# Optimization experiments

Hardware: AMD Instinct MI355X
Metric: run time of the kernel (lower is better)

## Reference

```python
import jax, jax.numpy as jnp
import numpy as np

B = 128          # batch size
N_KG = 500       # KG vertices
N = N_KG + 2     # + sensor node + zero target node
D = 1024         # embed_dim (hard-coded in forward)
H = 256          # gnn_hidden
E = 4000         # edges
EPS = 1e-5


def setup_inputs() -> dict:
    key = jax.random.key(0)
    ks = jax.random.split(key, 8)
    return {
        "sensor_batch": jax.random.normal(ks[0], (B, D), jnp.float32),
        "base_vertices": jax.random.normal(ks[1], (N_KG, D), jnp.float32),
        "edge_index": jax.random.randint(ks[2], (2, E), 0, N, jnp.int64),
        "W1": jax.random.normal(ks[3], (D, H), jnp.float32) * (1.0 / np.sqrt(D)),
        "b1": jnp.zeros((H,), jnp.float32),
        "gamma1": jnp.ones((H,), jnp.float32),
        "beta1": jnp.zeros((H,), jnp.float32),
        "W2": jax.random.normal(ks[4], (H, H), jnp.float32) * (1.0 / np.sqrt(H)),
        "b2": jnp.zeros((H,), jnp.float32),
        "gamma2": jnp.ones((H,), jnp.float32),
        "beta2": jnp.zeros((H,), jnp.float32),
        "W3": jax.random.normal(ks[5], (H, H), jnp.float32) * (1.0 / np.sqrt(H)),
        "b3": jnp.zeros((H,), jnp.float32),
        "gamma3": jnp.ones((H,), jnp.float32),
        "beta3": jnp.zeros((H,), jnp.float32),
    }


def _gcn_norm(edge_index):
    # add self loops, symmetric normalization D^{-1/2} A D^{-1/2}
    loops = jnp.arange(N, dtype=edge_index.dtype)
    src = jnp.concatenate([edge_index[0], loops])
    dst = jnp.concatenate([edge_index[1], loops])
    deg = jnp.zeros((N,), jnp.float32).at[dst].add(1.0)
    dinv = jnp.where(deg > 0, jax.lax.rsqrt(deg), 0.0)
    norm = dinv[src] * dinv[dst]   # [E+N]
    return src, dst, norm


def _gcn_conv(x, W, b, src, dst, norm):
    # x: [B, N, F_in] -> [B, N, F_out]
    h = jnp.einsum('bnf,fh->bnh', x, W)
    msg = h[:, src, :] * norm[None, :, None]            # gather + scale
    out = jnp.zeros_like(h).at[:, dst, :].add(msg)      # scatter-add
    return out + b


def _bn_elu(x, gamma, beta):
    # BatchNorm1d over flattened (B*N, H) in training mode, then ELU
    Bn, Nn, Hh = x.shape
    xf = x.reshape(Bn * Nn, Hh)
    mean = jnp.mean(xf, axis=0)
    var = jnp.mean(jnp.square(xf - mean), axis=0)  # biased, as in torch BN fwd
    y = (xf - mean) * jax.lax.rsqrt(var + EPS) * gamma + beta
    return jax.nn.elu(y).reshape(Bn, Nn, Hh)


def reference(sensor_batch, base_vertices, edge_index,
              W1, b1, gamma1, beta1,
              W2, b2, gamma2, beta2,
              W3, b3, gamma3, beta3):
    Bn = sensor_batch.shape[0]
    # x = [base_vertices; sensor_input; zeros] per batch element -> [B, N, D]
    base = jnp.broadcast_to(base_vertices[None], (Bn, N_KG, D))
    zeros = jnp.zeros((Bn, 1, D), sensor_batch.dtype)
    x = jnp.concatenate([base, sensor_batch[:, None, :], zeros], axis=1)

    src, dst, norm = _gcn_norm(edge_index)
    x = _bn_elu(_gcn_conv(x, W1, b1, src, dst, norm), gamma1, beta1)
    x = _bn_elu(_gcn_conv(x, W2, b2, src, dst, norm), gamma2, beta2)
    x = _bn_elu(_gcn_conv(x, W3, b3, src, dst, norm), gamma3, beta3)
    return x
```

## Files before the change

kernel.cpp:

```cpp
#include <hip/hip_runtime.h>
#include <cstdint>
#include <cstddef>

#define NNODES 502
#define NKG    500
#define NPAD   512
#define NEDGE  4000
#define NET    4502
#define BB     128
#define DD     1024
#define HH     256
#define MROWS  (BB*NNODES)
#define MT     65536
#define MCAT   628
#define EPITCH 136

typedef short short8 __attribute__((ext_vector_type(8)));
typedef float f32x4  __attribute__((ext_vector_type(4)));

__device__ __forceinline__ unsigned short f2bf(float f) {
  union { float f; unsigned int u; } v; v.f = f;
  unsigned int r = v.u + 0x7fffu + ((v.u >> 16) & 1u);
  return (unsigned short)(r >> 16);
}

__device__ __forceinline__ float bf2f(unsigned short u) {
  union { unsigned int u; float f; } v; v.u = ((unsigned int)u) << 16;
  return v.f;
}

__device__ __forceinline__ float elu(float y) {
  return (y > 0.f) ? y : (__expf(y) - 1.f);
}

__device__ __forceinline__ void stage16(const void* g, void* l) {
  __builtin_amdgcn_global_load_lds((__attribute__((address_space(1))) void*)g,
                                   (__attribute__((address_space(3))) void*)l, 16, 0, 0);
}

__device__ __forceinline__ void mfma16(f32x4& c, short8 a, short8 b) {
  asm volatile("v_mfma_f32_16x16x32_bf16 %0, %1, %2, %0" : "+v"(c) : "v"(a), "v"(b));
}

__device__ inline void get_edge(const int* __restrict__ e, int i, int i64mode,
                                int& src, int& dst) {
  if (i < NEDGE) {
    if (i64mode) { src = e[2*i]; dst = e[2*NEDGE + 2*i]; }
    else         { src = e[i];   dst = e[NEDGE + i]; }
  } else {
    src = dst = i - NEDGE;
  }
  src = min(max(src, 0), NNODES-1);
  dst = min(max(dst, 0), NNODES-1);
}

__device__ __forceinline__ int detect_mode(const int* __restrict__ e) {
  __shared__ int sflag;
  if (threadIdx.x == 0) sflag = 0;
  __syncthreads();
  if (e[2*threadIdx.x + 1] != 0) atomicOr(&sflag, 1);
  __syncthreads();
  return sflag == 0;
}

__global__ void deg_kernel(const int* __restrict__ e, int* __restrict__ deg) {
  int i64 = detect_mode(e);
  int i = blockIdx.x*256 + threadIdx.x;
  if (i >= NET) return;
  int src, dst; get_edge(e, i, i64, src, dst);
  atomicAdd(&deg[dst], 1);
}

__global__ void scan_kernel(const int* __restrict__ deg, float* __restrict__ dinv,
                            int* __restrict__ rp, int* __restrict__ cursor) {
  __shared__ int s[512];
  int t = threadIdx.x;
  int cnt = (t < NNODES) ? deg[t] : 0;
  s[t] = cnt;
  if (t < NNODES) dinv[t] = rsqrtf((float)cnt);
  __syncthreads();
  for (int off = 1; off < 512; off <<= 1) {
    int v = (t >= off) ? s[t-off] : 0;
    __syncthreads();
    s[t] += v;
    __syncthreads();
  }
  if (t == 0) rp[0] = 0;
  if (t < NNODES) { rp[t+1] = s[t]; cursor[t] = s[t] - cnt; }
}

__global__ void fillsdf_kernel(const int* __restrict__ e, const float* __restrict__ dinv,
                               int* __restrict__ cursor, int* __restrict__ colA,
                               float* __restrict__ valA, float* __restrict__ Sdf) {
  int i64 = detect_mode(e);
  int i = blockIdx.x*256 + threadIdx.x;
  if (i >= NET) return;
  int src, dst; get_edge(e, i, i64, src, dst);
  float v = dinv[src] * dinv[dst];
  int pos = atomicAdd(&cursor[dst], 1);
  colA[pos] = src;
  valA[pos] = v;
  atomicAdd(&Sdf[dst*NPAD + src], v);
}

__global__ void sdcvt_kernel(const float* __restrict__ Sdf, unsigned short* __restrict__ Sd) {
  int i = blockIdx.x*256 + threadIdx.x;
  Sd[i] = f2bf(Sdf[i]);
}

__global__ __launch_bounds__(256) void prep_kernel(
    const float* __restrict__ W1, const float* __restrict__ W2, const float* __restrict__ W3,
    const float* __restrict__ base, const float* __restrict__ sensor,
    unsigned short* __restrict__ Wt1, unsigned short* __restrict__ Wt2,
    unsigned short* __restrict__ Wt3, unsigned short* __restrict__ Xp1,
    float* __restrict__ hcatz) {
  int bid = blockIdx.x, tid = threadIdx.x;
  if (bid < 512) {
    const float* W = (bid & 256) ? W3 : W2;
    unsigned short* Wt = (bid & 256) ? Wt3 : Wt2;
    int n = bid & 255;
    Wt[n*HH + tid] = f2bf(W[(size_t)tid*HH + n]);
  } else if (bid < 768) {
    int n = bid - 512;
    for (int k = tid; k < DD; k += 256)
      Wt1[n*DD + k] = f2bf(W1[(size_t)k*HH + n]);
  } else if (bid < 1408) {
    int i = (bid - 768)*256 + tid;
    int r = i >> 8, c = (i & 255) * 4;
    float4 v = make_float4(0.f, 0.f, 0.f, 0.f);
    if (r < NKG) v = *(const float4*)&base[(size_t)r*DD + c];
    else if (r < MCAT) v = *(const float4*)&sensor[(size_t)(r-NKG)*DD + c];
    union { unsigned short u[4]; uint2 d; } p;
    p.u[0]=f2bf(v.x); p.u[1]=f2bf(v.y); p.u[2]=f2bf(v.z); p.u[3]=f2bf(v.w);
    *(uint2*)&Xp1[(size_t)r*DD + c] = p.d;
  } else {
    hcatz[(bid - 1408)*256 + tid] = 0.f;
  }
}

__global__ __launch_bounds__(256) void gemm1m_kernel(
    const unsigned short* __restrict__ Ag,
    const unsigned short* __restrict__ Bg,
    float* __restrict__ C) {
  __shared__ unsigned short As[128*32];
  __shared__ unsigned short Bs[128*32];
  int tid = threadIdx.x;
  int wave = tid >> 6, lane = tid & 63;
  int l15 = lane & 15, quad = lane >> 4;
  int wm = (wave & 1) * 64, wn = (wave >> 1) * 64;
  int row0 = blockIdx.y * 128, col0 = blockIdx.x * 128;
  int kbase = blockIdx.z * 256;
  f32x4 acc[4][4] = {};
  for (int k0 = kbase; k0 < kbase + 256; k0 += 32) {
#pragma unroll
    for (int q = 0; q < 2; ++q) {
      int c = wave*128 + q*64 + lane;
      stage16(Ag + (size_t)(row0 + (c>>2))*DD + k0 + (c&3)*8, As + c*8);
      stage16(Bg + (size_t)(col0 + (c>>2))*DD + k0 + (c&3)*8, Bs + c*8);
    }
    __syncthreads();
    short8 af[4], bfv[4];
#pragma unroll
    for (int i = 0; i < 4; ++i) {
      af[i]  = *(const short8*)(As + (wm + i*16 + l15)*32 + quad*8);
      bfv[i] = *(const short8*)(Bs + (wn + i*16 + l15)*32 + quad*8);
    }
#pragma unroll
    for (int mi = 0; mi < 4; ++mi)
#pragma unroll
      for (int ni = 0; ni < 4; ++ni)
        mfma16(acc[mi][ni], af[mi], bfv[ni]);
    __syncthreads();
  }
  asm volatile("s_nop 7\n\ts_nop 7" ::);
#pragma unroll
  for (int ni = 0; ni < 4; ++ni) {
    int n = col0 + wn + ni*16 + l15;
#pragma unroll
    for (int mi = 0; mi < 4; ++mi) {
      int m = row0 + wm + mi*16 + quad*4;
#pragma unroll
      for (int r = 0; r < 4; ++r)
        if (m + r < MCAT) atomicAdd(&C[(size_t)(m+r)*HH + n], acc[mi][ni][r]);
    }
  }
}

__global__ void ac_kernel(const int* __restrict__ rp, const int* __restrict__ colA,
                          const float* __restrict__ valA, const float* __restrict__ hcat,
                          float* __restrict__ Abuf, float* __restrict__ cbuf) {
  int n = blockIdx.x, h = threadIdx.x;
  int s = rp[n], e = rp[n+1];
  float acc = 0.f, cacc = 0.f;
  for (int t = s; t < e; ++t) {
    int cl = colA[t]; float v = valA[t];
    if (cl < NKG) acc += v * hcat[cl*HH + h];
    else if (cl == NKG) cacc += v;
  }
  Abuf[n*HH + h] = acc;
  if (h == 0) cbuf[n] = cacc;
}

__global__ __launch_bounds__(256) void bn1n_kernel(
    const float* __restrict__ Abuf, const float* __restrict__ cbuf,
    const float* __restrict__ hcat,
    float* __restrict__ sA1, float* __restrict__ sAA1, float* __restrict__ sAc1,
    float* __restrict__ scp, float* __restrict__ ssA, float* __restrict__ sssA) {
  int bid = blockIdx.x, h = threadIdx.x;
  if (bid < 32) {
    int n0 = bid*16, n1 = min(n0+16, NNODES);
    float sA = 0, sAA = 0, sAc = 0, sc = 0, scc = 0;
    for (int n = n0; n < n1; ++n) {
      float a = Abuf[n*HH + h]; float cn = cbuf[n];
      sA += a; sAA += a*a; sAc += a*cn; sc += cn; scc += cn*cn;
    }
    atomicAdd(&sA1[h], sA); atomicAdd(&sAA1[h], sAA); atomicAdd(&sAc1[h], sAc);
    if (h == 0) { atomicAdd(&scp[0], sc); atomicAdd(&scp[1], scc); }
  } else {
    int b0 = (bid-32)*16;
    float ss = 0, sss = 0;
    for (int b = b0; b < b0+16; ++b) {
      float v = hcat[(size_t)(NKG + b)*HH + h]; ss += v; sss += v*v;
    }
    atomicAdd(&ssA[h], ss); atomicAdd(&sssA[h], sss);
  }
}

__global__ void fin1_kernel(const float* __restrict__ sA1, const float* __restrict__ sAA1,
                            const float* __restrict__ sAc1, const float* __restrict__ scp,
                            const float* __restrict__ ssA, const float* __restrict__ sssA,
                            const float* __restrict__ gamma, const float* __restrict__ beta,
                            float* __restrict__ scale, float* __restrict__ shift) {
  int h = threadIdx.x;
  float sA = sA1[h], sAA = sAA1[h], sAc = sAc1[h];
  float sc = scp[0], scc = scp[1];
  float ss = ssA[h], sss = sssA[h];
  const float cnt = (float)MROWS;
  float mean = ((float)BB * sA + sc*ss) / cnt;
  float msq  = ((float)BB * sAA + 2.f*sAc*ss + scc*sss) / cnt;
  float var  = msq - mean*mean;
  float scl  = gamma[h] * rsqrtf(var + 1e-5f);
  scale[h] = scl; shift[h] = beta[h] - mean*scl;
}

__global__ __launch_bounds__(256) void x2_kernel(
    const float* __restrict__ Abuf, const float* __restrict__ cbuf,
    const float* __restrict__ hcat, const float* __restrict__ scale,
    const float* __restrict__ shift, unsigned short* __restrict__ Xb) {
  int idx = blockIdx.x*256 + threadIdx.x;
  int row = idx >> 6, h0 = (idx & 63)*4;
  int b = row >> 9, n = row & (NPAD-1);
  union { unsigned short u[4]; uint2 d; } p;
  p.d = make_uint2(0,0);
  if (n < NNODES) {
    float4 a  = *(const float4*)(Abuf + n*HH + h0);
    float4 s  = *(const float4*)(hcat + (size_t)(NKG + b)*HH + h0);
    float4 sc = *(const float4*)(scale + h0);
    float4 sh = *(const float4*)(shift + h0);
    float cn = cbuf[n];
    p.u[0] = f2bf(elu((a.x + cn*s.x)*sc.x + sh.x));
    p.u[1] = f2bf(elu((a.y + cn*s.y)*sc.y + sh.y));
    p.u[2] = f2bf(elu((a.z + cn*s.z)*sc.z + sh.z));
    p.u[3] = f2bf(elu((a.w + cn*s.w)*sc.w + sh.w));
  }
  *(uint2*)(Xb + (size_t)row*HH + h0) = p.d;
}

template<int FBN>
__global__ __launch_bounds__(256) void gemmT2_kernel(
    const unsigned short* __restrict__ Ag,
    const unsigned short* __restrict__ Bg,
    const float* __restrict__ sums, const float* __restrict__ ssqs,
    const float* __restrict__ gamma, const float* __restrict__ beta,
    unsigned short* __restrict__ Tt) {
  __shared__ __align__(16) unsigned short smem[25600];
  unsigned short* As = smem;
  unsigned short* Bs = smem + 8192;
  float* sclL = (float*)(smem + 24576);
  float* shfL = sclL + 256;
  int tid = threadIdx.x;
  int wave = tid >> 6, lane = tid & 63;
  int l15 = lane & 15, quad = lane >> 4;
  int wm = (wave & 1) * 64;
  int wnh = wave >> 1;
  int row0 = blockIdx.x * 128;
  if (FBN) {
    float mean = sums[tid] * (1.f/(float)MROWS);
    float var  = ssqs[tid] * (1.f/(float)MROWS) - mean*mean;
    float s = gamma[tid] * rsqrtf(var + 1e-5f);
    sclL[tid] = s; shfL[tid] = beta[tid] - mean*s;
    __syncthreads();
  }
  f32x4 acc[4][8] = {};
  for (int k0 = 0; k0 < HH; k0 += 64) {
#pragma unroll
    for (int q = 0; q < 8; ++q) {
      int c = q*256 + tid;
      int kb = c >> 10, rr = (c >> 2) & 255, j = c & 3;
      stage16(Bg + (size_t)rr*HH + k0 + kb*32 + j*8, Bs + c*8);
    }
#pragma unroll
    for (int q = 0; q < 4; ++q) {
      int c = q*256 + tid;
      int half = c >> 9, rr = (c >> 2) & 127, j = c & 3;
      int kk = k0 + half*32 + j*8;
      if (FBN) {
        union { unsigned short u[8]; uint4 d; } va, pa;
        va.d = *(const uint4*)(Ag + (size_t)(row0 + rr)*HH + kk);
#pragma unroll
        for (int t = 0; t < 8; ++t)
          pa.u[t] = f2bf(elu(bf2f(va.u[t])*sclL[kk+t] + shfL[kk+t]));
        *(uint4*)(As + c*8) = pa.d;
      } else {
        stage16(Ag + (size_t)(row0 + rr)*HH + kk, As + c*8);
      }
    }
    __syncthreads();
#pragma unroll
    for (int kb = 0; kb < 2; ++kb) {
      short8 af[4], bfv[8];
#pragma unroll
      for (int i = 0; i < 4; ++i)
        af[i] = *(const short8*)(As + kb*4096 + (wm + i*16 + l15)*32 + quad*8);
#pragma unroll
      for (int i = 0; i < 8; ++i)
        bfv[i] = *(const short8*)(Bs + kb*8192 + (wnh*128 + i*16 + l15)*32 + quad*8);
#pragma unroll
      for (int mi = 0; mi < 4; ++mi)
#pragma unroll
        for (int ni = 0; ni < 8; ++ni)
          mfma16(acc[mi][ni], af[mi], bfv[ni]);
    }
    __syncthreads();
  }
  asm volatile("s_nop 7\n\ts_nop 7" ::);
  int moff = (tid & 15)*8;
#pragma unroll
  for (int nh = 0; nh < 2; ++nh) {
    if (wnh == nh) {
#pragma unroll
      for (int ni = 0; ni < 8; ++ni) {
        int nl = ni*16 + l15;
#pragma unroll
        for (int mi = 0; mi < 4; ++mi) {
          int ml = wm + mi*16 + quad*4;
#pragma unroll
          for (int r = 0; r < 4; ++r)
            smem[nl*EPITCH + ml + r] = f2bf(acc[mi][ni][r]);
        }
      }
    }
    __syncthreads();
#pragma unroll
    for (int j = 0; j < 8; ++j) {
      int nr = (tid >> 4) + j*16;
      uint4 d = *(const uint4*)(smem + nr*EPITCH + moff);
      *(uint4*)(Tt + (size_t)(nh*128 + nr)*MT + row0 + moff) = d;
    }
    __syncthreads();
  }
}

__global__ __launch_bounds__(256) void gemmS2_kernel(
    const unsigned short* __restrict__ Sd,
    const unsigned short* __restrict__ Tt,
    unsigned short* __restrict__ Xbo,
    float* __restrict__ sums, float* __restrict__ ssqs) {
  __shared__ __align__(16) unsigned short smem[36864];
  unsigned short* As = smem;
  unsigned short* Bs = smem + 12288;
  int tid = threadIdx.x;
  int wave = tid >> 6, lane = tid & 63;
  int l15 = lane & 15, quad = lane >> 4;
  int wm = (wave & 1) * 64, wn = (wave >> 1) * 64;
  int id = blockIdx.x;
  int xcd = id & 7;
  int w = id >> 3;
  int y = w & 3;
  int g = (w >> 2) * 8 + xcd;
  int x = g >> 6;
  int b = (g & 63) * 2;
  int row0 = y * 128, col0 = x * 128;
  const unsigned short* Abase = Sd + (size_t)row0*NPAD;
  const unsigned short* Bbase = Tt + (size_t)col0*MT + (size_t)b*NPAD;
  int c0 = tid, c1 = 256 + tid;
  int r0 = c0 >> 2, o0 = (c0 & 3) * 8;
  int r1 = c1 >> 2, o1 = (c1 & 3) * 8;

  f32x4 acc[2][4][4] = {};
  auto STAGE = [&](int kn, int buf) {
    stage16(Abase + (size_t)r0*NPAD + kn + o0, As + buf*4096 + c0*8);
    stage16(Abase + (size_t)r1*NPAD + kn + o1, As + buf*4096 + c1*8);
#pragma unroll
    for (int q = 0; q < 4; ++q) {
      int c = q*256 + tid;
      int bb = c >> 9, cc = c & 511;
      int rr = cc >> 2, j = (cc & 3)*8;
      stage16(Bbase + (size_t)rr*MT + bb*NPAD + kn + j, Bs + buf*8192 + c*8);
    }
  };
  STAGE(0, 0);
  STAGE(32, 1);
  for (int t = 0; t < 16; ++t) {
    int cur = t % 3;
    if (t < 14) {
      STAGE((t+2)*32, (t+2) % 3);
      asm volatile("s_waitcnt vmcnt(12)" ::: "memory");
    } else if (t == 14) {
      asm volatile("s_waitcnt vmcnt(6)" ::: "memory");
    } else {
      asm volatile("s_waitcnt vmcnt(0)" ::: "memory");
    }
    __builtin_amdgcn_s_barrier();
    __builtin_amdgcn_sched_barrier(0);
    short8 af[4], bfv[2][4];
#pragma unroll
    for (int i = 0; i < 4; ++i)
      af[i] = *(const short8*)(As + cur*4096 + (wm + i*16 + l15)*32 + quad*8);
#pragma unroll
    for (int bb = 0; bb < 2; ++bb)
#pragma unroll
      for (int i = 0; i < 4; ++i)
        bfv[bb][i] = *(const short8*)(Bs + cur*8192 + bb*4096 + (wn + i*16 + l15)*32 + quad*8);
#pragma unroll
    for (int bb = 0; bb < 2; ++bb)
#pragma unroll
      for (int mi = 0; mi < 4; ++mi)
#pragma unroll
        for (int ni = 0; ni < 4; ++ni)
          mfma16(acc[bb][mi][ni], af[mi], bfv[bb][ni]);
    __builtin_amdgcn_sched_barrier(0);
    __builtin_amdgcn_s_barrier();
  }
  asm volatile("s_nop 7\n\ts_nop 7" ::);
  float ps[4] = {0,0,0,0}, pq[4] = {0,0,0,0};
#pragma unroll
  for (int bb = 0; bb < 2; ++bb)
#pragma unroll
    for (int ni = 0; ni < 4; ++ni)
#pragma unroll
      for (int mi = 0; mi < 4; ++mi)
#pragma unroll
        for (int r = 0; r < 4; ++r) {
          float v = acc[bb][mi][ni][r];
          ps[ni] += v; pq[ni] += v*v;
        }
  int noff = (tid & 15)*8;
#pragma unroll
  for (int bb = 0; bb < 2; ++bb) {
#pragma unroll
    for (int mi = 0; mi < 4; ++mi) {
      int ml = wm + mi*16 + quad*4;
#pragma unroll
      for (int ni = 0; ni < 4; ++ni) {
        int nl = wn + ni*16 + l15;
#pragma unroll
        for (int r = 0; r < 4; ++r)
          smem[(ml + r)*EPITCH + nl] = f2bf(acc[bb][mi][ni][r]);
      }
    }
    __syncthreads();
    unsigned short* Xrow = Xbo + (size_t)(b + bb)*NPAD*HH;
#pragma unroll
    for (int j = 0; j < 8; ++j) {
      int rr = (tid >> 4) + j*16;
      int node = row0 + rr;
      if (node < NNODES) {
        uint4 d = *(const uint4*)(smem + rr*EPITCH + noff);
        *(uint4*)(Xrow + (size_t)node*HH + col0 + noff) = d;
      }
    }
    __syncthreads();
  }
  float* red = (float*)smem;
  red[tid] = 0.f;
  __syncthreads();
#pragma unroll
  for (int ni = 0; ni < 4; ++ni) {
    int cl = wn + ni*16 + l15;
    atomicAdd(&red[cl], ps[ni]);
    atomicAdd(&red[128+cl], pq[ni]);
  }
  __syncthreads();
  if (tid < 128) atomicAdd(&sums[col0+tid], red[tid]);
  else atomicAdd(&ssqs[col0+tid-128], red[tid]);
}

__global__ void finalize_kernel(const float* __restrict__ sums, const float* __restrict__ ssqs,
                                const float* __restrict__ gamma, const float* __restrict__ beta,
                                float* __restrict__ scale, float* __restrict__ shift) {
  int h = threadIdx.x;
  const float cnt = (float)MROWS;
  float mean = sums[h] / cnt;
  float var  = ssqs[h] / cnt - mean*mean;
  float scl  = gamma[h] * rsqrtf(var + 1e-5f);
  scale[h] = scl; shift[h] = beta[h] - mean*scl;
}

__global__ __launch_bounds__(256) void bnout_kernel(
    const unsigned short* __restrict__ Xb, const float* __restrict__ scale,
    const float* __restrict__ shift, float* __restrict__ O) {
  int idx = blockIdx.x*256 + threadIdx.x;
  int row = idx >> 6, h0 = (idx & 63)*4;
  int b = row >> 9, n = row & (NPAD-1);
  if (n >= NNODES) return;
  union { unsigned short u[4]; uint2 d; } v;
  v.d = *(const uint2*)(Xb + (size_t)row*HH + h0);
  float4 sc = *(const float4*)(scale + h0);
  float4 sh = *(const float4*)(shift + h0);
  float4 o;
  o.x = elu(bf2f(v.u[0])*sc.x + sh.x);
  o.y = elu(bf2f(v.u[1])*sc.y + sh.y);
  o.z = elu(bf2f(v.u[2])*sc.z + sh.z);
  o.w = elu(bf2f(v.u[3])*sc.w + sh.w);
  *(float4*)(O + ((size_t)(b*NNODES + n)*HH + h0)) = o;
}

extern "C" void kernel_launch(void* const* d_in, const int* in_sizes, int n_in,
                              void* d_out, int out_size, void* d_ws, size_t ws_size,
                              hipStream_t stream) {
  const float* sensor = (const float*)d_in[0];
  const float* base   = (const float*)d_in[1];
  const int*   eidx   = (const int*)d_in[2];
  const float* W1 = (const float*)d_in[3];
  const float* g1 = (const float*)d_in[5];
  const float* be1= (const float*)d_in[6];
  const float* W2 = (const float*)d_in[7];
  const float* g2 = (const float*)d_in[9];
  const float* be2= (const float*)d_in[10];
  const float* W3 = (const float*)d_in[11];
  const float* g3 = (const float*)d_in[13];
  const float* be3= (const float*)d_in[14];

  char* ws = (char*)d_ws;
  int*   deg    = (int*)(ws + 0);
  float* sum2   = (float*)(ws + 2048);
  float* ssq2   = (float*)(ws + 3072);
  float* sum3   = (float*)(ws + 4096);
  float* ssq3   = (float*)(ws + 5120);
  float* cbuf   = (float*)(ws + 6144);
  int*   cursor = (int*)(ws + 8192);
  float* sA1    = (float*)(ws + 10496);
  float* sAA1   = (float*)(ws + 11520);
  float* sAc1   = (float*)(ws + 12544);
  float* scp    = (float*)(ws + 13568);
  float* ssA    = (float*)(ws + 13824);
  float* sssA   = (float*)(ws + 14848);
  float* dinv   = (float*)(ws + 16384);
  int*   rp     = (int*)(ws + 18432);
  int*   colA   = (int*)(ws + 20480);
  float* valA   = (float*)(ws + 40960);
  float* scale1 = (float*)(ws + 61440);
  float* shift1 = (float*)(ws + 62464);
  float* scale3 = (float*)(ws + 65536);
  float* shift3 = (float*)(ws + 66560);
  float* Abuf   = (float*)(ws + 67584);
  float* hcat   = (float*)(ws + 581632);
  unsigned short* Wt2 = (unsigned short*)(ws + 1224704);
  unsigned short* Wt3 = (unsigned short*)(ws + 1355776);
  unsigned short* Sd  = (unsigned short*)(ws + 1486848);
  unsigned short* Xb  = (unsigned short*)(ws + 2011136);
  unsigned short* Tt  = (unsigned short*)(ws + 35565568UL);
  unsigned short* Xp1 = (unsigned short*)(ws + 35565568UL);
  unsigned short* Wt1 = (unsigned short*)(ws + 35565568UL + 1310720);
  float* out = (float*)d_out;
  float* Sdf = (float*)d_out;

  hipMemsetAsync(ws, 0, 16384, stream);
  hipMemsetAsync(d_out, 0, NPAD*NPAD*4, stream);
  deg_kernel<<<(NET+255)/256, 256, 0, stream>>>(eidx, deg);
  scan_kernel<<<1, 512, 0, stream>>>(deg, dinv, rp, cursor);
  fillsdf_kernel<<<(NET+255)/256, 256, 0, stream>>>(eidx, dinv, cursor, colA, valA, Sdf);
  sdcvt_kernel<<<(NPAD*NPAD)/256, 256, 0, stream>>>(Sdf, Sd);
  prep_kernel<<<2036, 256, 0, stream>>>(W1, W2, W3, base, sensor, Wt1, Wt2, Wt3, Xp1, hcat);

  gemm1m_kernel<<<dim3(2, 5, 4), 256, 0, stream>>>(Xp1, Wt1, hcat);
  ac_kernel<<<NNODES, 256, 0, stream>>>(rp, colA, valA, hcat, Abuf, cbuf);
  bn1n_kernel<<<40, 256, 0, stream>>>(Abuf, cbuf, hcat, sA1, sAA1, sAc1, scp, ssA, sssA);
  fin1_kernel<<<1, 256, 0, stream>>>(sA1, sAA1, sAc1, scp, ssA, sssA, g1, be1, scale1, shift1);
  x2_kernel<<<(MT*64)/256, 256, 0, stream>>>(Abuf, cbuf, hcat, scale1, shift1, Xb);

  gemmT2_kernel<0><<<MT/128, 256, 0, stream>>>(Xb, Wt2, sum2, ssq2, g2, be2, Tt);
  gemmS2_kernel<<<512, 256, 0, stream>>>(Sd, Tt, Xb, sum2, ssq2);
  gemmT2_kernel<1><<<MT/128, 256, 0, stream>>>(Xb, Wt3, sum2, ssq2, g2, be2, Tt);
  gemmS2_kernel<<<512, 256, 0, stream>>>(Sd, Tt, Xb, sum3, ssq3);
  finalize_kernel<<<1, 256, 0, stream>>>(sum3, ssq3, g3, be3, scale3, shift3);
  bnout_kernel<<<(MT*64)/256, 256, 0, stream>>>(Xb, scale3, shift3, out);
}
```

Before: 294.4 us.

## Triple-buffer the T-GEMM K-loop with async prefetch and manual waitcnts

```diff
diff --git a/kernel.cpp b/kernel.cpp
--- a/kernel.cpp
+++ b/kernel.cpp
@@ -267,17 +267,16 @@
 }
 
 template<int FBN>
-__global__ __launch_bounds__(256) void gemmT2_kernel(
+__global__ __launch_bounds__(256) void gemmT3_kernel(
     const unsigned short* __restrict__ Ag,
     const unsigned short* __restrict__ Bg,
     const float* __restrict__ sums, const float* __restrict__ ssqs,
     const float* __restrict__ gamma, const float* __restrict__ beta,
     unsigned short* __restrict__ Tt) {
-  __shared__ __align__(16) unsigned short smem[25600];
+  __shared__ __align__(16) unsigned short smem[36864];
+  __shared__ float sclL[256], shfL[256];
   unsigned short* As = smem;
-  unsigned short* Bs = smem + 8192;
-  float* sclL = (float*)(smem + 24576);
-  float* shfL = sclL + 256;
+  unsigned short* Bs = smem + 12288;
   int tid = threadIdx.x;
   int wave = tid >> 6, lane = tid & 63;
   int l15 = lane & 15, quad = lane >> 4;
@@ -291,47 +290,100 @@
     sclL[tid] = s; shfL[tid] = beta[tid] - mean*s;
     __syncthreads();
   }
-  f32x4 acc[4][8] = {};
-  for (int k0 = 0; k0 < HH; k0 += 64) {
-#pragma unroll
-    for (int q = 0; q < 8; ++q) {
-      int c = q*256 + tid;
-      int kb = c >> 10, rr = (c >> 2) & 255, j = c & 3;
-      stage16(Bg + (size_t)rr*HH + k0 + kb*32 + j*8, Bs + c*8);
-    }
+  int c0 = tid, c1 = 256 + tid;
+  int r0 = c0 >> 2, o0 = (c0 & 3) * 8;
+  int r1 = c1 >> 2, o1 = (c1 & 3) * 8;
+  const unsigned short* A0 = Ag + (size_t)(row0 + r0)*HH + o0;
+  const unsigned short* A1 = Ag + (size_t)(row0 + r1)*HH + o1;
+
+  auto XF = [&](uint4 v, int kk) -> uint4 {
+    union { unsigned short u[8]; uint4 d; } va, pa;
+    va.d = v;
+#pragma unroll
+    for (int s = 0; s < 8; ++s)
+      pa.u[s] = f2bf(elu(bf2f(va.u[s])*sclL[kk+s] + shfL[kk+s]));
+    return pa.d;
+  };
+  auto STAGE_B = [&](int kn, int buf) {
 #pragma unroll
     for (int q = 0; q < 4; ++q) {
       int c = q*256 + tid;
-      int half = c >> 9, rr = (c >> 2) & 127, j = c & 3;
-      int kk = k0 + half*32 + j*8;
-      if (FBN) {
-        union { unsigned short u[8]; uint4 d; } va, pa;
-        va.d = *(const uint4*)(Ag + (size_t)(row0 + rr)*HH + kk);
-#pragma unroll
-        for (int t = 0; t < 8; ++t)
-          pa.u[t] = f2bf(elu(bf2f(va.u[t])*sclL[kk+t] + shfL[kk+t]));
-        *(uint4*)(As + c*8) = pa.d;
+      int rr = c >> 2, j = (c & 3)*8;
+      stage16(Bg + (size_t)rr*HH + kn + j, Bs + buf*8192 + c*8);
+    }
+  };
+
+  f32x4 acc[4][8] = {};
+  if (FBN) {
+    uint4 p00 = *(const uint4*)(A0);
+    uint4 p01 = *(const uint4*)(A1);
+    uint4 p10 = *(const uint4*)(A0 + 32);
+    uint4 p11 = *(const uint4*)(A1 + 32);
+    STAGE_B(0, 0);
+    STAGE_B(32, 1);
+    *(uint4*)(As + c0*8)        = XF(p00, o0);
+    *(uint4*)(As + c1*8)        = XF(p01, o1);
+    *(uint4*)(As + 4096 + c0*8) = XF(p10, 32 + o0);
+    *(uint4*)(As + 4096 + c1*8) = XF(p11, 32 + o1);
+    asm volatile("s_waitcnt lgkmcnt(0)" ::: "memory");
+  } else {
+    stage16(A0, As + c0*8);
+    stage16(A1, As + c1*8);
+    STAGE_B(0, 0);
+    stage16(A0 + 32, As + 4096 + c0*8);
+    stage16(A1 + 32, As + 4096 + c1*8);
+    STAGE_B(32, 1);
+  }
+  uint4 na0, na1;
+#pragma unroll
+  for (int t = 0; t < 8; ++t) {
+    int cur = t % 3;
+    int nxt2 = (t + 2) % 3;
+    if (FBN) {
+      if (t >= 1 && t <= 6) {
+        na0 = *(const uint4*)(A0 + (t+1)*32);
+        na1 = *(const uint4*)(A1 + (t+1)*32);
+      }
+      if (t < 6) STAGE_B((t+2)*32, nxt2);
+      if (t == 0)      asm volatile("s_waitcnt vmcnt(8)"  ::: "memory");
+      else if (t <= 5) asm volatile("s_waitcnt vmcnt(10)" ::: "memory");
+      else if (t == 6) asm volatile("s_waitcnt vmcnt(6)"  ::: "memory");
+      else             asm volatile("s_waitcnt vmcnt(0)"  ::: "memory");
+    } else {
+      if (t < 6) {
+        stage16(A0 + (t+2)*32, As + nxt2*4096 + c0*8);
+        stage16(A1 + (t+2)*32, As + nxt2*4096 + c1*8);
+        STAGE_B((t+2)*32, nxt2);
+        asm volatile("s_waitcnt vmcnt(12)" ::: "memory");
+      } else if (t == 6) {
+        asm volatile("s_waitcnt vmcnt(6)" ::: "memory");
       } else {
-        stage16(Ag + (size_t)(row0 + rr)*HH + kk, As + c*8);
+        asm volatile("s_waitcnt vmcnt(0)" ::: "memory");
       }
     }
-    __syncthreads();
-#pragma unroll
-    for (int kb = 0; kb < 2; ++kb) {
-      short8 af[4], bfv[8];
-#pragma unroll
-      for (int i = 0; i < 4; ++i)
-        af[i] = *(const short8*)(As + kb*4096 + (wm + i*16 + l15)*32 + quad*8);
-#pragma unroll
-      for (int i = 0; i < 8; ++i)
-        bfv[i] = *(const short8*)(Bs + kb*8192 + (wnh*128 + i*16 + l15)*32 + quad*8);
-#pragma unroll
-      for (int mi = 0; mi < 4; ++mi)
-#pragma unroll
-        for (int ni = 0; ni < 8; ++ni)
-          mfma16(acc[mi][ni], af[mi], bfv[ni]);
-    }
-    __syncthreads();
+    __builtin_amdgcn_s_barrier();
+    __builtin_amdgcn_sched_barrier(0);
+    short8 af[4], bfv[8];
+#pragma unroll
+    for (int i = 0; i < 4; ++i)
+      af[i] = *(const short8*)(As + cur*4096 + (wm + i*16 + l15)*32 + quad*8);
+#pragma unroll
+    for (int i = 0; i < 8; ++i)
+      bfv[i] = *(const short8*)(Bs + cur*8192 + (wnh*128 + i*16 + l15)*32 + quad*8);
+#pragma unroll
+    for (int mi = 0; mi < 4; ++mi)
+#pragma unroll
+      for (int ni = 0; ni < 8; ++ni)
+        mfma16(acc[mi][ni], af[mi], bfv[ni]);
+    if (FBN && t >= 1 && t <= 6) {
+      int nb = (t + 1) % 3;
+      int kk = (t + 1) * 32;
+      *(uint4*)(As + nb*4096 + c0*8) = XF(na0, kk + o0);
+      *(uint4*)(As + nb*4096 + c1*8) = XF(na1, kk + o1);
+      asm volatile("s_waitcnt lgkmcnt(0)" ::: "memory");
+    }
+    __builtin_amdgcn_sched_barrier(0);
+    __builtin_amdgcn_s_barrier();
   }
   asm volatile("s_nop 7\n\ts_nop 7" ::);
   int moff = (tid & 15)*8;
@@ -580,9 +632,9 @@
   fin1_kernel<<<1, 256, 0, stream>>>(sA1, sAA1, sAc1, scp, ssA, sssA, g1, be1, scale1, shift1);
   x2_kernel<<<(MT*64)/256, 256, 0, stream>>>(Abuf, cbuf, hcat, scale1, shift1, Xb);
 
-  gemmT2_kernel<0><<<MT/128, 256, 0, stream>>>(Xb, Wt2, sum2, ssq2, g2, be2, Tt);
+  gemmT3_kernel<0><<<MT/128, 256, 0, stream>>>(Xb, Wt2, sum2, ssq2, g2, be2, Tt);
   gemmS2_kernel<<<512, 256, 0, stream>>>(Sd, Tt, Xb, sum2, ssq2);
-  gemmT2_kernel<1><<<MT/128, 256, 0, stream>>>(Xb, Wt3, sum2, ssq2, g2, be2, Tt);
+  gemmT3_kernel<1><<<MT/128, 256, 0, stream>>>(Xb, Wt3, sum2, ssq2, g2, be2, Tt);
   gemmS2_kernel<<<512, 256, 0, stream>>>(Sd, Tt, Xb, sum3, ssq3);
   finalize_kernel<<<1, 256, 0, stream>>>(sum3, ssq3, g3, be3, scale3, shift3);
   bnout_kernel<<<(MT*64)/256, 256, 0, stream>>>(Xb, scale3, shift3, out);
```

Result: no change. 289.0 us (median of 2 runs) (-1.8%).
